# Performance work log

Hardware: AMD Instinct MI355X
Metric: run time of the kernel (lower is better)

## Reference

```python
import jax, jax.numpy as jnp
import numpy as np

EPS = 1e-5  # torch BatchNorm1d default eps


def setup_inputs() -> dict:
    key = jax.random.key(0)
    ks = jax.random.split(key, 8)
    F, P = 32, 64            # frames, peds per frame
    B = F * P                # batch = 2048
    E, H, M, D = 64, 128, 512, 1024  # embed, h_dim, pool_mlp_dim, bottleneck
    starts = np.arange(F, dtype=np.int64) * P
    seq_start_end = jnp.asarray(np.stack([starts, starts + P], axis=1))
    inp = {
        "curr_h_states": jax.random.normal(ks[0], (1, B, H), dtype=jnp.float32),
        "curr_pos": jax.random.normal(ks[1], (B, 2), dtype=jnp.float32),
        "seq_start_end": seq_start_end,
        # embedding: Linear(2, E)
        "We": jax.random.normal(ks[2], (2, E), dtype=jnp.float32) * 0.5,
        "be": jnp.zeros((E,), dtype=jnp.float32),
        # mlp layer 1: Linear(E+H, M) + BN(M)
        "W1": jax.random.normal(ks[3], (E + H, M), dtype=jnp.float32) * 0.05,
        "b1": jnp.zeros((M,), dtype=jnp.float32),
        "g1": jnp.ones((M,), dtype=jnp.float32),
        "beta1": jnp.zeros((M,), dtype=jnp.float32),
        # mlp layer 2: Linear(M, D) + BN(D)
        "W2": jax.random.normal(ks[4], (M, D), dtype=jnp.float32) * 0.04,
        "b2": jnp.zeros((D,), dtype=jnp.float32),
        "g2": jnp.ones((D,), dtype=jnp.float32),
        "beta2": jnp.zeros((D,), dtype=jnp.float32),
        # BN running stats (eval mode)
        "rm1": jnp.zeros((M,), dtype=jnp.float32),
        "rv1": jnp.ones((M,), dtype=jnp.float32),
        "rm2": jnp.zeros((D,), dtype=jnp.float32),
        "rv2": jnp.ones((D,), dtype=jnp.float32),
    }
    return inp


def _bn(x, g, beta, rm, rv):
    return g * (x - rm) * jax.lax.rsqrt(rv + EPS) + beta


def reference(curr_h_states, curr_pos, seq_start_end, We, be, W1, b1, g1, beta1,
              W2, b2, g2, beta2, rm1, rv1, rm2, rv2):
    # Equal-size frames: vectorize the per-frame Python loop via a reshape.
    F = seq_start_end.shape[0]
    B = curr_h_states.shape[1]
    P = B // F
    h = curr_h_states[0].reshape(F, P, -1)      # (F, P, H)
    pos = curr_pos.reshape(F, P, 2)             # (F, P, 2)
    # rel_pos[f, i, j] = pos[f, j] - pos[f, i]  (repeat minus repeat_interleave)
    rel = pos[:, None, :, :] - pos[:, :, None, :]          # (F, P, P, 2)
    emb = rel @ We + be                                     # (F, P, P, E)
    h_rep = jnp.broadcast_to(h[:, None, :, :], (F, P, P, h.shape[-1]))
    x = jnp.concatenate([emb, h_rep], axis=-1)              # (F, P, P, E+H)
    x = jax.nn.relu(_bn(x @ W1 + b1, g1, beta1, rm1, rv1))  # (F, P, P, M)
    x = jax.nn.relu(_bn(x @ W2 + b2, g2, beta2, rm2, rv2))  # (F, P, P, D)
    pool_h = x.max(axis=2)                                  # max over j -> (F, P, D)
    return pool_h.reshape(B, -1)                            # (B, D)
```

## Files before the change

### kernel.cpp

```cpp
#include <hip/hip_runtime.h>
#include <hip/hip_bf16.h>
#include <stdint.h>

#define EPS_BN 1e-5f

constexpr int Fn = 32;
constexpr int Pn = 64;
constexpr int Bn = 2048;
constexpr int Hn = 128;
constexpr int En = 64;
constexpr int Mn = 512;
constexpr int Dn = 1024;

using bf16x8 = __attribute__((ext_vector_type(8))) short;
using f32x4  = __attribute__((ext_vector_type(4))) float;

static __device__ __forceinline__ float    bcf(uint32_t u) { return __builtin_bit_cast(float, u); }
static __device__ __forceinline__ uint32_t bcu(float f)    { return __builtin_bit_cast(uint32_t, f); }
static __device__ __forceinline__ unsigned short bfbits(float f) {
  return __builtin_bit_cast(unsigned short, __float2bfloat16(f));
}

__global__ void prep0(const float* __restrict__ We, const float* __restrict__ be,
                      const float* __restrict__ W1, const float* __restrict__ b1,
                      float* __restrict__ Wr, float* __restrict__ cb) {
  int m = threadIdx.x;
  float w0 = 0.f, w1 = 0.f, c = 0.f;
  for (int e = 0; e < En; ++e) {
    float w = W1[e * Mn + m];
    w0 += We[e] * w;
    w1 += We[En + e] * w;
    c  += be[e] * w;
  }
  Wr[m]      = w0;
  Wr[Mn + m] = w1;
  cb[m]      = c + b1[m];
}

__global__ void prep1(const float* __restrict__ hs, const float* __restrict__ pos,
                      const float* __restrict__ W1,
                      const float* __restrict__ g1, const float* __restrict__ beta1,
                      const float* __restrict__ rm1, const float* __restrict__ rv1,
                      const float* __restrict__ Wr, const float* __restrict__ cb,
                      __hip_bfloat16* __restrict__ Agb, __hip_bfloat16* __restrict__ Qgb) {
  int rb = blockIdx.x * 8;
  int m  = threadIdx.x;
  __shared__ float hsh[8 * Hn];
  __shared__ float psh[16];
  for (int idx = m; idx < 8 * Hn; idx += Mn) hsh[idx] = hs[rb * Hn + idx];
  if (m < 16) psh[m] = pos[rb * 2 + m];
  __syncthreads();

  float s  = g1[m] * rsqrtf(rv1[m] + EPS_BN);
  float tt = beta1[m] - rm1[m] * s;
  float wr0 = Wr[m], wr1 = Wr[Mn + m], c = cb[m];

  float acc[8];
#pragma unroll
  for (int ri = 0; ri < 8; ++ri) acc[ri] = c;
  for (int e = 0; e < Hn; ++e) {
    float w = W1[(En + e) * Mn + m];
#pragma unroll
    for (int ri = 0; ri < 8; ++ri) acc[ri] += hsh[ri * Hn + e] * w;
  }
#pragma unroll
  for (int ri = 0; ri < 8; ++ri) {
    float q = psh[ri * 2] * wr0 + psh[ri * 2 + 1] * wr1;
    Agb[(rb + ri) * Mn + m] = __float2bfloat16((acc[ri] + q) * s + tt);
    Qgb[(rb + ri) * Mn + m] = __float2bfloat16(q * s);
  }
}

__global__ void prep2(const float* __restrict__ W2, const float* __restrict__ g2,
                      const float* __restrict__ beta2, const float* __restrict__ rm2,
                      const float* __restrict__ rv2, const float* __restrict__ b2,
                      uint4* __restrict__ W2f, float* __restrict__ c2) {
  __shared__ float tile[64][65];
  int d0 = blockIdx.x * 64;
  int k0 = blockIdx.y * 64;
  int t  = threadIdx.x;
  int col  = t & 63;
  int row4 = t >> 6;
#pragma unroll
  for (int rr = 0; rr < 16; ++rr) {
    int row = rr * 4 + row4;
    tile[row][col] = W2[(k0 + row) * Dn + d0 + col];
  }
  __syncthreads();

  int lane = t & 63, sel = t >> 6;
  int dl = sel * 16 + (lane & 15);
  int d  = d0 + dl;
  float s = g2[d] * rsqrtf(rv2[d] + EPS_BN);
#pragma unroll
  for (int kcl = 0; kcl < 2; ++kcl) {
    int kb = kcl * 32 + (lane >> 4) * 8;
    uint32_t w[4];
#pragma unroll
    for (int h = 0; h < 4; ++h) {
      unsigned short u0 = bfbits(tile[kb + 2 * h][dl] * s);
      unsigned short u1 = bfbits(tile[kb + 2 * h + 1][dl] * s);
      w[h] = (uint32_t)u0 | ((uint32_t)u1 << 16);
    }
    int ntile = (d0 >> 4) + sel;
    int kc    = (k0 >> 5) + kcl;
    W2f[(ntile * 16 + kc) * 64 + lane] = (uint4){w[0], w[1], w[2], w[3]};
  }
  if (blockIdx.y == 0 && t < 64) {
    int dd = d0 + t;
    float ss = g2[dd] * rsqrtf(rv2[dd] + EPS_BN);
    c2[dd] = b2[dd] * ss + beta2[dd] - rm2[dd] * ss;
  }
}

__launch_bounds__(256, 3)
__global__ void gemm_pool(const __hip_bfloat16* __restrict__ Agb,
                          const __hip_bfloat16* __restrict__ Qgb,
                          const uint4* __restrict__ W2f,
                          const float* __restrict__ c2, float* __restrict__ out) {
  __shared__ unsigned short As[2][4096];
  __shared__ unsigned short Bs[2][4096];

  int ct = blockIdx.x;
  int rt = blockIdx.y;
  int f  = rt >> 5;
  int i0 = (rt & 31) * 2;

  int t    = threadIdx.x;
  int lane = t & 63;
  int g    = t >> 6;
  int wm   = g & 1;
  int wn   = g >> 1;

  int jA    = g * 16 + (lane & 15);
  int koct8 = (lane >> 4) * 8;

  const uint4* aP  = (const uint4*)(Agb + (f * Pn + jA) * Mn + koct8);
  const uint4* q0P = (const uint4*)(Qgb + (f * Pn + i0) * Mn + koct8);
  const uint4* q1P = (const uint4*)(Qgb + (f * Pn + i0 + 1) * Mn + koct8);
  const uint4* b0P = W2f + ((ct * 8 + g) * 16) * 64 + lane;
  const uint4* b1P = W2f + ((ct * 8 + g + 4) * 16) * 64 + lane;

  uint4 rA  = aP[0];
  uint4 rQ0 = q0P[0];
  uint4 rQ1 = q1P[0];
  uint4 rB0 = b0P[0];
  uint4 rB1 = b1P[0];

  f32x4 acc[4][4];
#pragma unroll
  for (int mt = 0; mt < 4; ++mt)
#pragma unroll
    for (int nt = 0; nt < 4; ++nt) acc[mt][nt] = (f32x4){0.f, 0.f, 0.f, 0.f};

  int slot0 = (g * 64 + lane) * 8;
  int slot1 = ((g + 4) * 64 + lane) * 8;

#pragma unroll 2
  for (int kc = 0; kc < 16; ++kc) {
    int p = kc & 1;
    uint4 x0, x1;
#pragma unroll
    for (int w = 0; w < 4; ++w) {
      uint32_t aw  = ((const uint32_t*)&rA)[w];
      float alo = bcf(aw << 16), ahi = bcf(aw & 0xFFFF0000u);
      uint32_t q0w = ((const uint32_t*)&rQ0)[w];
      uint32_t q1w = ((const uint32_t*)&rQ1)[w];
      float x0lo = fmaxf(alo - bcf(q0w << 16), 0.f);
      float x0hi = fmaxf(ahi - bcf(q0w & 0xFFFF0000u), 0.f);
      float x1lo = fmaxf(alo - bcf(q1w << 16), 0.f);
      float x1hi = fmaxf(ahi - bcf(q1w & 0xFFFF0000u), 0.f);
      ((uint32_t*)&x0)[w] = (bcu(x0lo) >> 16) | (bcu(x0hi) & 0xFFFF0000u);
      ((uint32_t*)&x1)[w] = (bcu(x1lo) >> 16) | (bcu(x1hi) & 0xFFFF0000u);
    }
    *(uint4*)&As[p][slot0] = x0;
    *(uint4*)&As[p][slot1] = x1;
    *(uint4*)&Bs[p][slot0] = rB0;
    *(uint4*)&Bs[p][slot1] = rB1;

    asm volatile("s_waitcnt lgkmcnt(0)\n\ts_barrier" ::: "memory");

    int kn = (kc < 15) ? kc + 1 : 15;
    rA  = aP[kn * 4];
    rQ0 = q0P[kn * 4];
    rQ1 = q1P[kn * 4];
    rB0 = b0P[kn * 64];
    rB1 = b1P[kn * 64];

    bf16x8 af[4], bg[4];
#pragma unroll
    for (int mt = 0; mt < 4; ++mt)
      af[mt] = *(const bf16x8*)&As[p][((wm * 4 + mt) * 64 + lane) * 8];
#pragma unroll
    for (int nt = 0; nt < 4; ++nt)
      bg[nt] = *(const bf16x8*)&Bs[p][((wn * 4 + nt) * 64 + lane) * 8];
#pragma unroll
    for (int mt = 0; mt < 4; ++mt)
#pragma unroll
      for (int nt = 0; nt < 4; ++nt)
        acc[mt][nt] = __builtin_amdgcn_mfma_f32_16x16x32_bf16(af[mt], bg[nt],
                                                              acc[mt][nt], 0, 0, 0);
  }

  int d0 = ct * 128;
  float red[4];
#pragma unroll
  for (int nt = 0; nt < 4; ++nt) {
    int d = d0 + wn * 64 + nt * 16 + (lane & 15);
    float c2v = c2[d];
    float mx = 0.f;
#pragma unroll
    for (int mt = 0; mt < 4; ++mt)
#pragma unroll
      for (int rg = 0; rg < 4; ++rg)
        mx = fmaxf(mx, acc[mt][nt][rg] + c2v);
    mx = fmaxf(mx, __shfl_xor(mx, 16));
    mx = fmaxf(mx, __shfl_xor(mx, 32));
    red[nt] = mx;
  }
  int nts = lane >> 4;
  float val = (nts == 0) ? red[0] : (nts == 1) ? red[1] : (nts == 2) ? red[2] : red[3];
  int row_out = f * Pn + i0 + wm;
  out[row_out * Dn + d0 + wn * 64 + nts * 16 + (lane & 15)] = val;
}

extern "C" void kernel_launch(void* const* d_in, const int* in_sizes, int n_in,
                              void* d_out, int out_size, void* d_ws, size_t ws_size,
                              hipStream_t stream) {
  const float* hs    = (const float*)d_in[0];
  const float* pos   = (const float*)d_in[1];
  const float* We    = (const float*)d_in[3];
  const float* be    = (const float*)d_in[4];
  const float* W1    = (const float*)d_in[5];
  const float* b1    = (const float*)d_in[6];
  const float* g1    = (const float*)d_in[7];
  const float* beta1 = (const float*)d_in[8];
  const float* W2    = (const float*)d_in[9];
  const float* b2    = (const float*)d_in[10];
  const float* g2    = (const float*)d_in[11];
  const float* beta2 = (const float*)d_in[12];
  const float* rm1   = (const float*)d_in[13];
  const float* rv1   = (const float*)d_in[14];
  const float* rm2   = (const float*)d_in[15];
  const float* rv2   = (const float*)d_in[16];

  char* ws = (char*)d_ws;
  float* Wr  = (float*)(ws + 0);
  float* cb  = (float*)(ws + 4096);
  float* c2  = (float*)(ws + 6144);
  __hip_bfloat16* Agb = (__hip_bfloat16*)(ws + 10240);
  __hip_bfloat16* Qgb = (__hip_bfloat16*)(ws + 10240 + 2097152);
  uint4* W2f = (uint4*)(ws + 10240 + 2 * 2097152);
  float* out = (float*)d_out;

  prep0<<<1, Mn, 0, stream>>>(We, be, W1, b1, Wr, cb);
  prep2<<<dim3(Dn / 64, Mn / 64), 256, 0, stream>>>(W2, g2, beta2, rm2, rv2, b2, W2f, c2);
  prep1<<<Bn / 8, Mn, 0, stream>>>(hs, pos, W1, g1, beta1, rm1, rv1, Wr, cb, Agb, Qgb);
  gemm_pool<<<dim3(Dn / 128, (Bn * Pn) / 128), 256, 0, stream>>>(Agb, Qgb, W2f, c2, out);
}
```

Before: 277.4 us.

## Merge prep kernels and restructure GEMM to register A-fragments with LDS DMA for B

The three preprocessing kernels become one launch: each block recomputes the embedding-folded W1 terms itself and blocks are split by index between the layer-1 and W2-packing work. The main GEMM no longer stages the A operand in shared memory. Each wave builds its bf16 A fragment directly in registers and multiplies it against all 8 N-tiles, while B is copied with global_load_lds DMA into double-buffered LDS. The max-pool reduction now goes through shared memory across waves, and the bias add and relu are moved after the max. This cuts LDS traffic and launch count, at the cost of more accumulator registers, redundant W1 work per prep block, and an extra barrier for the reduction.

```diff
diff --git a/kernel.cpp b/kernel.cpp
--- a/kernel.cpp
+++ b/kernel.cpp
@@ -21,95 +21,83 @@
   return __builtin_bit_cast(unsigned short, __float2bfloat16(f));
 }
 
-__global__ void prep0(const float* __restrict__ We, const float* __restrict__ be,
-                      const float* __restrict__ W1, const float* __restrict__ b1,
-                      float* __restrict__ Wr, float* __restrict__ cb) {
-  int m = threadIdx.x;
-  float w0 = 0.f, w1 = 0.f, c = 0.f;
-  for (int e = 0; e < En; ++e) {
-    float w = W1[e * Mn + m];
-    w0 += We[e] * w;
-    w1 += We[En + e] * w;
-    c  += be[e] * w;
-  }
-  Wr[m]      = w0;
-  Wr[Mn + m] = w1;
-  cb[m]      = c + b1[m];
-}
-
-__global__ void prep1(const float* __restrict__ hs, const float* __restrict__ pos,
-                      const float* __restrict__ W1,
-                      const float* __restrict__ g1, const float* __restrict__ beta1,
-                      const float* __restrict__ rm1, const float* __restrict__ rv1,
-                      const float* __restrict__ Wr, const float* __restrict__ cb,
-                      __hip_bfloat16* __restrict__ Agb, __hip_bfloat16* __restrict__ Qgb) {
-  int rb = blockIdx.x * 8;
-  int m  = threadIdx.x;
-  __shared__ float hsh[8 * Hn];
-  __shared__ float psh[16];
-  for (int idx = m; idx < 8 * Hn; idx += Mn) hsh[idx] = hs[rb * Hn + idx];
-  if (m < 16) psh[m] = pos[rb * 2 + m];
-  __syncthreads();
-
-  float s  = g1[m] * rsqrtf(rv1[m] + EPS_BN);
-  float tt = beta1[m] - rm1[m] * s;
-  float wr0 = Wr[m], wr1 = Wr[Mn + m], c = cb[m];
-
-  float acc[8];
-#pragma unroll
-  for (int ri = 0; ri < 8; ++ri) acc[ri] = c;
-  for (int e = 0; e < Hn; ++e) {
-    float w = W1[(En + e) * Mn + m];
-#pragma unroll
-    for (int ri = 0; ri < 8; ++ri) acc[ri] += hsh[ri * Hn + e] * w;
-  }
-#pragma unroll
-  for (int ri = 0; ri < 8; ++ri) {
-    float q = psh[ri * 2] * wr0 + psh[ri * 2 + 1] * wr1;
-    Agb[(rb + ri) * Mn + m] = __float2bfloat16((acc[ri] + q) * s + tt);
-    Qgb[(rb + ri) * Mn + m] = __float2bfloat16(q * s);
-  }
-}
-
-__global__ void prep2(const float* __restrict__ W2, const float* __restrict__ g2,
-                      const float* __restrict__ beta2, const float* __restrict__ rm2,
-                      const float* __restrict__ rv2, const float* __restrict__ b2,
-                      uint4* __restrict__ W2f, float* __restrict__ c2) {
-  __shared__ float tile[64][65];
-  int d0 = blockIdx.x * 64;
-  int k0 = blockIdx.y * 64;
-  int t  = threadIdx.x;
-  int col  = t & 63;
-  int row4 = t >> 6;
-#pragma unroll
-  for (int rr = 0; rr < 16; ++rr) {
-    int row = rr * 4 + row4;
-    tile[row][col] = W2[(k0 + row) * Dn + d0 + col];
-  }
-  __syncthreads();
-
-  int lane = t & 63, sel = t >> 6;
-  int dl = sel * 16 + (lane & 15);
-  int d  = d0 + dl;
-  float s = g2[d] * rsqrtf(rv2[d] + EPS_BN);
-#pragma unroll
-  for (int kcl = 0; kcl < 2; ++kcl) {
+static __device__ __forceinline__ void dma16(const uint4* g, uint4* l) {
+  __builtin_amdgcn_global_load_lds(
+      (const __attribute__((address_space(1))) unsigned int*)g,
+      (__attribute__((address_space(3))) unsigned int*)l, 16, 0, 0);
+}
+
+__global__ void prep_all(const float* __restrict__ hs, const float* __restrict__ pos,
+                         const float* __restrict__ We, const float* __restrict__ be,
+                         const float* __restrict__ W1, const float* __restrict__ b1,
+                         const float* __restrict__ g1, const float* __restrict__ beta1,
+                         const float* __restrict__ rm1, const float* __restrict__ rv1,
+                         const float* __restrict__ W2, const float* __restrict__ b2,
+                         const float* __restrict__ g2, const float* __restrict__ beta2,
+                         const float* __restrict__ rm2, const float* __restrict__ rv2,
+                         __hip_bfloat16* __restrict__ Agb, __hip_bfloat16* __restrict__ Qgb,
+                         uint4* __restrict__ W2f, float* __restrict__ c2) {
+  __shared__ float smem[64 * 65];
+  int bid = blockIdx.x, t = threadIdx.x;
+  if (bid < 256) {
+    int rb = bid * 8, m = t;
+    float* hsh = smem;
+    float* psh = smem + 1024;
+    for (int idx = t; idx < 8 * Hn; idx += 512) hsh[idx] = hs[rb * Hn + idx];
+    if (t < 16) psh[t] = pos[rb * 2 + t];
+    __syncthreads();
+    float w0 = 0.f, w1 = 0.f, c = 0.f;
+    for (int e = 0; e < En; ++e) {
+      float w = W1[e * Mn + m];
+      w0 += We[e] * w; w1 += We[En + e] * w; c += be[e] * w;
+    }
+    c += b1[m];
+    float s  = g1[m] * rsqrtf(rv1[m] + EPS_BN);
+    float tt = beta1[m] - rm1[m] * s;
+    float acc[8];
+#pragma unroll
+    for (int ri = 0; ri < 8; ++ri) acc[ri] = c;
+    for (int e = 0; e < Hn; ++e) {
+      float w = W1[(En + e) * Mn + m];
+#pragma unroll
+      for (int ri = 0; ri < 8; ++ri) acc[ri] += hsh[ri * Hn + e] * w;
+    }
+#pragma unroll
+    for (int ri = 0; ri < 8; ++ri) {
+      float q = psh[ri * 2] * w0 + psh[ri * 2 + 1] * w1;
+      Agb[(rb + ri) * Mn + m] = __float2bfloat16((acc[ri] + q) * s + tt);
+      Qgb[(rb + ri) * Mn + m] = __float2bfloat16(q * s);
+    }
+  } else {
+    int b2i = bid - 256;
+    int d0 = (b2i & 15) * 64, k0 = (b2i >> 4) * 64;
+    int col = t & 63, row8 = t >> 6;
+#pragma unroll
+    for (int rr = 0; rr < 8; ++rr) {
+      int row = rr * 8 + row8;
+      smem[row * 65 + col] = W2[(k0 + row) * Dn + d0 + col];
+    }
+    __syncthreads();
+    int lane = t & 63, q8 = t >> 6;
+    int sel = q8 & 3, kcl = q8 >> 2;
+    int dl = sel * 16 + (lane & 15), d = d0 + dl;
+    float sf = g2[d] * rsqrtf(rv2[d] + EPS_BN);
     int kb = kcl * 32 + (lane >> 4) * 8;
-    uint32_t w[4];
+    uint32_t wd[4];
 #pragma unroll
     for (int h = 0; h < 4; ++h) {
-      unsigned short u0 = bfbits(tile[kb + 2 * h][dl] * s);
-      unsigned short u1 = bfbits(tile[kb + 2 * h + 1][dl] * s);
-      w[h] = (uint32_t)u0 | ((uint32_t)u1 << 16);
+      uint32_t u0 = bfbits(smem[(kb + 2 * h) * 65 + dl] * sf);
+      uint32_t u1 = bfbits(smem[(kb + 2 * h + 1) * 65 + dl] * sf);
+      wd[h] = u0 | (u1 << 16);
     }
     int ntile = (d0 >> 4) + sel;
     int kc    = (k0 >> 5) + kcl;
-    W2f[(ntile * 16 + kc) * 64 + lane] = (uint4){w[0], w[1], w[2], w[3]};
-  }
-  if (blockIdx.y == 0 && t < 64) {
-    int dd = d0 + t;
-    float ss = g2[dd] * rsqrtf(rv2[dd] + EPS_BN);
-    c2[dd] = b2[dd] * ss + beta2[dd] - rm2[dd] * ss;
+    W2f[(ntile * 16 + kc) * 64 + lane] = (uint4){wd[0], wd[1], wd[2], wd[3]};
+    if (k0 == 0 && t < 64) {
+      int dd = d0 + t;
+      float ss = g2[dd] * rsqrtf(rv2[dd] + EPS_BN);
+      c2[dd] = b2[dd] * ss + beta2[dd] - rm2[dd] * ss;
+    }
   }
 }
 
@@ -118,110 +106,96 @@
                           const __hip_bfloat16* __restrict__ Qgb,
                           const uint4* __restrict__ W2f,
                           const float* __restrict__ c2, float* __restrict__ out) {
-  __shared__ unsigned short As[2][4096];
-  __shared__ unsigned short Bs[2][4096];
+  __shared__ uint4 Bs[2][512];
+  __shared__ float red_s[4][2][128];
 
   int ct = blockIdx.x;
   int rt = blockIdx.y;
-  int f  = rt >> 5;
-  int i0 = (rt & 31) * 2;
-
-  int t    = threadIdx.x;
-  int lane = t & 63;
-  int g    = t >> 6;
-  int wm   = g & 1;
-  int wn   = g >> 1;
-
-  int jA    = g * 16 + (lane & 15);
-  int koct8 = (lane >> 4) * 8;
-
-  const uint4* aP  = (const uint4*)(Agb + (f * Pn + jA) * Mn + koct8);
-  const uint4* q0P = (const uint4*)(Qgb + (f * Pn + i0) * Mn + koct8);
-  const uint4* q1P = (const uint4*)(Qgb + (f * Pn + i0 + 1) * Mn + koct8);
-  const uint4* b0P = W2f + ((ct * 8 + g) * 16) * 64 + lane;
-  const uint4* b1P = W2f + ((ct * 8 + g + 4) * 16) * 64 + lane;
-
-  uint4 rA  = aP[0];
-  uint4 rQ0 = q0P[0];
-  uint4 rQ1 = q1P[0];
-  uint4 rB0 = b0P[0];
-  uint4 rB1 = b1P[0];
-
-  f32x4 acc[4][4];
-#pragma unroll
-  for (int mt = 0; mt < 4; ++mt)
-#pragma unroll
-    for (int nt = 0; nt < 4; ++nt) acc[mt][nt] = (f32x4){0.f, 0.f, 0.f, 0.f};
-
-  int slot0 = (g * 64 + lane) * 8;
-  int slot1 = ((g + 4) * 64 + lane) * 8;
-
-#pragma unroll 2
+  int f = rt >> 5, i0 = (rt & 31) * 2;
+  int t = threadIdx.x, lane = t & 63, w = t >> 6;
+
+  int jr = w * 16 + (lane & 15);
+  int ko = (lane >> 4) * 8;
+
+  const uint4* aP  = (const uint4*)(Agb + (f * Pn + jr) * Mn + ko);
+  const uint4* q0P = (const uint4*)(Qgb + (f * Pn + i0) * Mn + ko);
+  const uint4* q1P = (const uint4*)(Qgb + (f * Pn + i0 + 1) * Mn + ko);
+  const uint4* bS0 = W2f + ((ct * 8 + 2 * w) * 16) * 64 + lane;
+  const uint4* bS1 = W2f + ((ct * 8 + 2 * w + 1) * 16) * 64 + lane;
+
+  dma16(bS0, &Bs[0][(2 * w) * 64]);
+  dma16(bS1, &Bs[0][(2 * w + 1) * 64]);
+  uint4 rA = aP[0], rQ0 = q0P[0], rQ1 = q1P[0];
+
+  f32x4 acc0[8], acc1[8];
+#pragma unroll
+  for (int nt = 0; nt < 8; ++nt) {
+    acc0[nt] = (f32x4){0.f, 0.f, 0.f, 0.f};
+    acc1[nt] = (f32x4){0.f, 0.f, 0.f, 0.f};
+  }
+
+#pragma unroll
   for (int kc = 0; kc < 16; ++kc) {
     int p = kc & 1;
+    __syncthreads();
+
+    bf16x8 bg[8];
+#pragma unroll
+    for (int nt = 0; nt < 8; ++nt)
+      bg[nt] = *(const bf16x8*)&Bs[p][nt * 64 + lane];
+
+    uint4 nA = rA, nQ0 = rQ0, nQ1 = rQ1;
+    if (kc < 15) {
+      dma16(bS0 + (kc + 1) * 64, &Bs[p ^ 1][(2 * w) * 64]);
+      dma16(bS1 + (kc + 1) * 64, &Bs[p ^ 1][(2 * w + 1) * 64]);
+      nA  = aP[(kc + 1) * 4];
+      nQ0 = q0P[(kc + 1) * 4];
+      nQ1 = q1P[(kc + 1) * 4];
+    }
+
     uint4 x0, x1;
 #pragma unroll
-    for (int w = 0; w < 4; ++w) {
-      uint32_t aw  = ((const uint32_t*)&rA)[w];
-      float alo = bcf(aw << 16), ahi = bcf(aw & 0xFFFF0000u);
-      uint32_t q0w = ((const uint32_t*)&rQ0)[w];
-      uint32_t q1w = ((const uint32_t*)&rQ1)[w];
+    for (int v = 0; v < 4; ++v) {
+      uint32_t aw  = ((const uint32_t*)&rA)[v];
+      uint32_t q0w = ((const uint32_t*)&rQ0)[v];
+      uint32_t q1w = ((const uint32_t*)&rQ1)[v];
+      float alo = bcf(aw << 16), ahi = bcf(aw);
       float x0lo = fmaxf(alo - bcf(q0w << 16), 0.f);
-      float x0hi = fmaxf(ahi - bcf(q0w & 0xFFFF0000u), 0.f);
+      float x0hi = fmaxf(ahi - bcf(q0w), 0.f);
       float x1lo = fmaxf(alo - bcf(q1w << 16), 0.f);
-      float x1hi = fmaxf(ahi - bcf(q1w & 0xFFFF0000u), 0.f);
-      ((uint32_t*)&x0)[w] = (bcu(x0lo) >> 16) | (bcu(x0hi) & 0xFFFF0000u);
-      ((uint32_t*)&x1)[w] = (bcu(x1lo) >> 16) | (bcu(x1hi) & 0xFFFF0000u);
-    }
-    *(uint4*)&As[p][slot0] = x0;
-    *(uint4*)&As[p][slot1] = x1;
-    *(uint4*)&Bs[p][slot0] = rB0;
-    *(uint4*)&Bs[p][slot1] = rB1;
-
-    asm volatile("s_waitcnt lgkmcnt(0)\n\ts_barrier" ::: "memory");
-
-    int kn = (kc < 15) ? kc + 1 : 15;
-    rA  = aP[kn * 4];
-    rQ0 = q0P[kn * 4];
-    rQ1 = q1P[kn * 4];
-    rB0 = b0P[kn * 64];
-    rB1 = b1P[kn * 64];
-
-    bf16x8 af[4], bg[4];
-#pragma unroll
-    for (int mt = 0; mt < 4; ++mt)
-      af[mt] = *(const bf16x8*)&As[p][((wm * 4 + mt) * 64 + lane) * 8];
-#pragma unroll
-    for (int nt = 0; nt < 4; ++nt)
-      bg[nt] = *(const bf16x8*)&Bs[p][((wn * 4 + nt) * 64 + lane) * 8];
-#pragma unroll
-    for (int mt = 0; mt < 4; ++mt)
-#pragma unroll
-      for (int nt = 0; nt < 4; ++nt)
-        acc[mt][nt] = __builtin_amdgcn_mfma_f32_16x16x32_bf16(af[mt], bg[nt],
-                                                              acc[mt][nt], 0, 0, 0);
-  }
-
-  int d0 = ct * 128;
-  float red[4];
-#pragma unroll
-  for (int nt = 0; nt < 4; ++nt) {
-    int d = d0 + wn * 64 + nt * 16 + (lane & 15);
-    float c2v = c2[d];
-    float mx = 0.f;
-#pragma unroll
-    for (int mt = 0; mt < 4; ++mt)
-#pragma unroll
-      for (int rg = 0; rg < 4; ++rg)
-        mx = fmaxf(mx, acc[mt][nt][rg] + c2v);
-    mx = fmaxf(mx, __shfl_xor(mx, 16));
-    mx = fmaxf(mx, __shfl_xor(mx, 32));
-    red[nt] = mx;
-  }
-  int nts = lane >> 4;
-  float val = (nts == 0) ? red[0] : (nts == 1) ? red[1] : (nts == 2) ? red[2] : red[3];
-  int row_out = f * Pn + i0 + wm;
-  out[row_out * Dn + d0 + wn * 64 + nts * 16 + (lane & 15)] = val;
+      float x1hi = fmaxf(ahi - bcf(q1w), 0.f);
+      ((uint32_t*)&x0)[v] = __builtin_amdgcn_perm(bcu(x0hi), bcu(x0lo), 0x07060302u);
+      ((uint32_t*)&x1)[v] = __builtin_amdgcn_perm(bcu(x1hi), bcu(x1lo), 0x07060302u);
+    }
+    bf16x8 af0 = __builtin_bit_cast(bf16x8, x0);
+    bf16x8 af1 = __builtin_bit_cast(bf16x8, x1);
+
+#pragma unroll
+    for (int nt = 0; nt < 8; ++nt) {
+      acc0[nt] = __builtin_amdgcn_mfma_f32_16x16x32_bf16(af0, bg[nt], acc0[nt], 0, 0, 0);
+      acc1[nt] = __builtin_amdgcn_mfma_f32_16x16x32_bf16(af1, bg[nt], acc1[nt], 0, 0, 0);
+    }
+    rA = nA; rQ0 = nQ0; rQ1 = nQ1;
+  }
+
+#pragma unroll
+  for (int nt = 0; nt < 8; ++nt) {
+    float m0 = fmaxf(fmaxf(acc0[nt][0], acc0[nt][1]), fmaxf(acc0[nt][2], acc0[nt][3]));
+    float m1 = fmaxf(fmaxf(acc1[nt][0], acc1[nt][1]), fmaxf(acc1[nt][2], acc1[nt][3]));
+    m0 = fmaxf(m0, __shfl_xor(m0, 16));
+    m0 = fmaxf(m0, __shfl_xor(m0, 32));
+    m1 = fmaxf(m1, __shfl_xor(m1, 16));
+    m1 = fmaxf(m1, __shfl_xor(m1, 32));
+    if (lane < 16) {
+      red_s[w][0][nt * 16 + lane] = m0;
+      red_s[w][1][nt * 16 + lane] = m1;
+    }
+  }
+  __syncthreads();
+  int is = t >> 7, dl = t & 127;
+  float v = fmaxf(fmaxf(red_s[0][is][dl], red_s[1][is][dl]),
+                  fmaxf(red_s[2][is][dl], red_s[3][is][dl]));
+  out[(f * Pn + i0 + is) * Dn + ct * 128 + dl] = fmaxf(v + c2[ct * 128 + dl], 0.f);
 }
 
 extern "C" void kernel_launch(void* const* d_in, const int* in_sizes, int n_in,
@@ -245,16 +219,13 @@
   const float* rv2   = (const float*)d_in[16];
 
   char* ws = (char*)d_ws;
-  float* Wr  = (float*)(ws + 0);
-  float* cb  = (float*)(ws + 4096);
-  float* c2  = (float*)(ws + 6144);
-  __hip_bfloat16* Agb = (__hip_bfloat16*)(ws + 10240);
-  __hip_bfloat16* Qgb = (__hip_bfloat16*)(ws + 10240 + 2097152);
-  uint4* W2f = (uint4*)(ws + 10240 + 2 * 2097152);
+  float* c2 = (float*)(ws + 0);
+  __hip_bfloat16* Agb = (__hip_bfloat16*)(ws + 4096);
+  __hip_bfloat16* Qgb = (__hip_bfloat16*)(ws + 4096 + 2097152);
+  uint4* W2f = (uint4*)(ws + 4096 + 2 * 2097152);
   float* out = (float*)d_out;
 
-  prep0<<<1, Mn, 0, stream>>>(We, be, W1, b1, Wr, cb);
-  prep2<<<dim3(Dn / 64, Mn / 64), 256, 0, stream>>>(W2, g2, beta2, rm2, rv2, b2, W2f, c2);
-  prep1<<<Bn / 8, Mn, 0, stream>>>(hs, pos, W1, g1, beta1, rm1, rv1, Wr, cb, Agb, Qgb);
+  prep_all<<<384, 512, 0, stream>>>(hs, pos, We, be, W1, b1, g1, beta1, rm1, rv1,
+                                    W2, b2, g2, beta2, rm2, rv2, Agb, Qgb, W2f, c2);
   gemm_pool<<<dim3(Dn / 128, (Bn * Pn) / 128), 256, 0, stream>>>(Agb, Qgb, W2f, c2, out);
 }
```

New measurement: 281.8 us. About the same (+1.6%).
